# Kernel tuning notes

Hardware: AMD Instinct MI355X
Metric: run time of the kernel (lower is better)

## Reference

```python
import jax, jax.numpy as jnp
import numpy as np

B, S, D_IN, D_OUT, N, R = 8, 4096, 1280, 1280, 4, 16


def setup_inputs() -> dict:
    key = jax.random.key(0)
    ks = jax.random.split(key, 7)
    x = jax.random.normal(ks[0], (B, S, D_IN), dtype=jnp.float32)
    W = jax.random.normal(ks[1], (D_OUT, D_IN), dtype=jnp.float32) * 0.02
    bias = jax.random.normal(ks[2], (D_OUT,), dtype=jnp.float32) * 0.02
    A = jax.random.normal(ks[3], (N, R, D_IN), dtype=jnp.float32) * 0.02
    Bw = jax.random.normal(ks[4], (N, D_OUT, R), dtype=jnp.float32) * 0.02
    scalings = jax.random.uniform(ks[5], (N,), dtype=jnp.float32)
    masks = jax.random.uniform(ks[6], (N, S), dtype=jnp.float32)
    # normalize masks to sum ~1 per position, per docstring
    masks = masks / jnp.sum(masks, axis=0, keepdims=True)
    return {"x": x, "W": W, "bias": bias, "A": A, "Bw": Bw,
            "scalings": scalings, "masks": masks}


def reference(x, W, bias, A, Bw, scalings, masks):
    # base linear: y = x @ W^T + b
    base = jnp.einsum('bsd,od->bso', x, W) + bias
    # batched LoRA branches: h = x @ A_i^T  (b,s,n,r)
    h = jnp.einsum('bsd,nrd->bsnr', x, A)
    # lora_out_i = h @ B_i^T  (b,s,n,o)
    lora = jnp.einsum('bsnr,nor->bsno', h, Bw)
    # weighted sum over subjects: scaling_i * mask_i(pos)
    lora_sum = jnp.einsum('bsno,n,ns->bso', lora, scalings, masks)
    return base + lora_sum
```

## Files before the change

kernel.cpp:

```cpp
#include <hip/hip_runtime.h>
#include <hip/hip_bf16.h>
#include <stdint.h>

#define S_LEN   4096
#define DIN     1280
#define DOUT    1280
#define N_LORA  4
#define R_LORA  16
#define M_TOT   32768
#define KC      (DIN + N_LORA*R_LORA)
#define NR      64

typedef __attribute__((ext_vector_type(4))) float floatx4;
typedef __attribute__((ext_vector_type(8))) short shortx8;

typedef union { uint4 u; shortx8 s; } punx8;

static __device__ __forceinline__ unsigned short bf16_rne(float f) {
    union { float f; unsigned u; } v; v.f = f;
    unsigned u = v.u;
    u += 0x7fffu + ((u >> 16) & 1u);
    return (unsigned short)(u >> 16);
}

static __device__ __forceinline__ void async16(const unsigned short* g, unsigned short* l) {
    __builtin_amdgcn_global_load_lds(
        (const __attribute__((address_space(1))) unsigned int*)g,
        (__attribute__((address_space(3))) unsigned int*)l, 16, 0, 0);
}

static __device__ __forceinline__ uint4 cvt8(const float* src) {
    const float4* p = (const float4*)src;
    float4 a = p[0], b = p[1];
    uint4 o;
    o.x = (unsigned)bf16_rne(a.x) | ((unsigned)bf16_rne(a.y) << 16);
    o.y = (unsigned)bf16_rne(a.z) | ((unsigned)bf16_rne(a.w) << 16);
    o.z = (unsigned)bf16_rne(b.x) | ((unsigned)bf16_rne(b.y) << 16);
    o.w = (unsigned)bf16_rne(b.z) | ((unsigned)bf16_rne(b.w) << 16);
    return o;
}

__global__ __launch_bounds__(256) void k_convert_x(const float* __restrict__ x,
                                                   unsigned short* __restrict__ xb) {
    size_t e = ((size_t)blockIdx.x * 256 + threadIdx.x) * 8;
    *(uint4*)(xb + e) = cvt8(x + e);
}

__global__ __launch_bounds__(256) void k_build_wcat(const float* __restrict__ W,
                                                    const float* __restrict__ Bw,
                                                    unsigned short* __restrict__ Wcat) {
    int i = blockIdx.x * 256 + threadIdx.x;
    int e = i * 8;
    int o = e / KC;
    int c = e - o * KC;
    const float* src;
    if (c < DIN) {
        src = W + o * DIN + c;
    } else {
        int j = c - DIN;
        int n = j >> 4, r = j & 15;
        src = Bw + (n * DOUT + o) * R_LORA + r;
    }
    *(uint4*)(Wcat + o * KC + c) = cvt8(src);
}

__global__ __launch_bounds__(256) void k_convert_abp(const float* __restrict__ A,
                                                     unsigned short* __restrict__ Abp) {
    int step = blockIdx.x;
    int t = threadIdx.x;
    int ct = t >> 6, lane = t & 63;
    int mi = lane & 15, kq = lane >> 4;
    const float* src = A + (ct * 16 + mi) * DIN + step * 32 + kq * 8;
    *(uint4*)(Abp + ((size_t)(step * 4 + ct) * 64 + lane) * 8) = cvt8(src);
}

__global__ __launch_bounds__(1024) void k_lora_g(const unsigned short* __restrict__ xb,
                                                 const unsigned short* __restrict__ Abp,
                                                 const float* __restrict__ scalings,
                                                 const float* __restrict__ masks,
                                                 unsigned short* __restrict__ g) {
    __shared__ float hs[4][64][64];
    int tid = threadIdx.x;
    int wave = tid >> 6, lane = tid & 63;
    int kg = wave >> 2, wv = wave & 3;
    int mi = lane & 15, kq = lane >> 4;
    int m0 = blockIdx.x * 64;

    const unsigned short* xrow = xb + (size_t)(m0 + wv * 16 + mi) * DIN;

    floatx4 acc[4] = {};
    for (int s = 0; s < 10; ++s) {
        int step = kg * 10 + s;
        int k = step * 32 + kq * 8;
        shortx8 xf = *(const shortx8*)(xrow + k);
#pragma unroll
        for (int ct = 0; ct < 4; ++ct) {
            shortx8 bfr = *(const shortx8*)(Abp + ((size_t)(step * 4 + ct) * 64 + lane) * 8);
            acc[ct] = __builtin_amdgcn_mfma_f32_16x16x32_bf16(xf, bfr, acc[ct], 0, 0, 0);
        }
    }
#pragma unroll
    for (int ct = 0; ct < 4; ++ct)
#pragma unroll
        for (int reg = 0; reg < 4; ++reg)
            hs[kg][wv * 16 + kq * 4 + reg][ct * 16 + mi] = acc[ct][reg];
    __syncthreads();

    int r = tid >> 4;
    int c0 = (tid & 15) * 4;
    float4 s0 = *(const float4*)&hs[0][r][c0];
    float4 s1 = *(const float4*)&hs[1][r][c0];
    float4 s2 = *(const float4*)&hs[2][r][c0];
    float4 s3 = *(const float4*)&hs[3][r][c0];
    int n = c0 >> 4;
    int m = m0 + r;
    float wgt = scalings[n] * masks[n * S_LEN + (m & (S_LEN - 1))];
    float v0 = (s0.x + s1.x + s2.x + s3.x) * wgt;
    float v1 = (s0.y + s1.y + s2.y + s3.y) * wgt;
    float v2 = (s0.z + s1.z + s2.z + s3.z) * wgt;
    float v3 = (s0.w + s1.w + s2.w + s3.w) * wgt;
    uint2 packed;
    packed.x = (unsigned)bf16_rne(v0) | ((unsigned)bf16_rne(v1) << 16);
    packed.y = (unsigned)bf16_rne(v2) | ((unsigned)bf16_rne(v3) << 16);
    *(uint2*)(g + (size_t)m * NR + c0) = packed;
}

__global__ __launch_bounds__(256) void k_main_gemm(const unsigned short* __restrict__ xb,
                                                   const unsigned short* __restrict__ g,
                                                   const unsigned short* __restrict__ Wcat,
                                                   const float* __restrict__ bias,
                                                   float* __restrict__ out) {
    __shared__ unsigned short As[128 * 32];
    __shared__ unsigned short Bs[128 * 32];
    int tid = threadIdx.x;
    int wave = tid >> 6, lane = tid & 63;

    int bx = blockIdx.x;
    int xcd = bx & 7;
    int slot = bx >> 3;
    int rb = xcd * 32 + slot / 10;
    int cb = slot % 10;
    int m0 = rb * 128, n0 = cb * 128;

    int wr = wave >> 1, wc = wave & 1;
    int mi = lane & 15, kq = lane >> 4;

    int c0 = tid, c1 = tid + 256;
    int ar0 = c0 >> 2, ak0 = (c0 & 3) * 8;
    int ar1 = c1 >> 2, ak1 = (c1 & 3) * 8;

    floatx4 acc[4][4] = {};

    for (int k0 = 0; k0 < KC; k0 += 32) {
        if (k0 < DIN) {
            async16(xb + (size_t)(m0 + ar0) * DIN + k0 + ak0, As + c0 * 8);
            async16(xb + (size_t)(m0 + ar1) * DIN + k0 + ak1, As + c1 * 8);
        } else {
            async16(g + (size_t)(m0 + ar0) * NR + (k0 - DIN) + ak0, As + c0 * 8);
            async16(g + (size_t)(m0 + ar1) * NR + (k0 - DIN) + ak1, As + c1 * 8);
        }
        async16(Wcat + (size_t)(n0 + ar0) * KC + k0 + ak0, Bs + c0 * 8);
        async16(Wcat + (size_t)(n0 + ar1) * KC + k0 + ak1, Bs + c1 * 8);
        __syncthreads();
        shortx8 af[4], bf[4];
#pragma unroll
        for (int t = 0; t < 4; ++t) {
            af[t] = *(const shortx8*)(As + (wr * 64 + t * 16 + mi) * 32 + kq * 8);
            bf[t] = *(const shortx8*)(Bs + (wc * 64 + t * 16 + mi) * 32 + kq * 8);
        }
#pragma unroll
        for (int i = 0; i < 4; ++i)
#pragma unroll
            for (int j = 0; j < 4; ++j)
                acc[i][j] = __builtin_amdgcn_mfma_f32_16x16x32_bf16(af[i], bf[j], acc[i][j], 0, 0, 0);
        __syncthreads();
    }

#pragma unroll
    for (int j = 0; j < 4; ++j) {
        int col = n0 + wc * 64 + j * 16 + mi;
        float bv = bias[col];
#pragma unroll
        for (int i = 0; i < 4; ++i) {
            int rbase = m0 + wr * 64 + i * 16 + kq * 4;
#pragma unroll
            for (int reg = 0; reg < 4; ++reg) {
                out[(size_t)(rbase + reg) * DOUT + col] = acc[i][j][reg] + bv;
            }
        }
    }
}

extern "C" void kernel_launch(void* const* d_in, const int* in_sizes, int n_in,
                              void* d_out, int out_size, void* d_ws, size_t ws_size,
                              hipStream_t stream) {
    const float* x     = (const float*)d_in[0];
    const float* W     = (const float*)d_in[1];
    const float* bias  = (const float*)d_in[2];
    const float* A     = (const float*)d_in[3];
    const float* Bw    = (const float*)d_in[4];
    const float* scal  = (const float*)d_in[5];
    const float* masks = (const float*)d_in[6];
    float* out = (float*)d_out;

    unsigned short* xb   = (unsigned short*)d_ws;
    unsigned short* g    = xb + (size_t)M_TOT * DIN;
    unsigned short* Wcat = g + (size_t)M_TOT * NR;
    unsigned short* Abp  = Wcat + (size_t)DOUT * KC;

    k_convert_x<<<(M_TOT * DIN) / (8 * 256), 256, 0, stream>>>(x, xb);
    k_build_wcat<<<(DOUT * KC) / (8 * 256), 256, 0, stream>>>(W, Bw, Wcat);
    k_convert_abp<<<DIN / 32, 256, 0, stream>>>(A, Abp);
    k_lora_g<<<M_TOT / 64, 1024, 0, stream>>>(xb, Abp, scal, masks, g);
    k_main_gemm<<<(M_TOT / 128) * (DOUT / 128), 256, 0, stream>>>(xb, g, Wcat, bias, out);
}
```

Before: 465.8 us.

## Restructure main GEMM into double-buffered 256x128 tiles with swizzled LDS and split pipeline

The main GEMM moves from a 128x128 tile with 256 threads and single-buffered K=32 steps to a 256x128 tile with 512 threads, K=64 steps, and double-buffered LDS. Async global-to-LDS loads for the next tiles are issued between split MFMA phases, with explicit vmcnt waits, raw barriers and setprio, so memory traffic overlaps compute. LDS rows are XOR-swizzled to avoid bank conflicts on fragment reads. The larger per-block tile raises data reuse, but it also increases LDS use and register pressure, and the hand-written wait counts are fragile.

```diff
diff --git a/kernel.cpp b/kernel.cpp
--- a/kernel.cpp
+++ b/kernel.cpp
@@ -10,6 +10,7 @@
 #define M_TOT   32768
 #define KC      (DIN + N_LORA*R_LORA)
 #define NR      64
+#define NT      21
 
 typedef __attribute__((ext_vector_type(4))) float floatx4;
 typedef __attribute__((ext_vector_type(8))) short shortx8;
@@ -38,6 +39,13 @@
     o.z = (unsigned)bf16_rne(b.x) | ((unsigned)bf16_rne(b.y) << 16);
     o.w = (unsigned)bf16_rne(b.z) | ((unsigned)bf16_rne(b.w) << 16);
     return o;
+}
+
+#define VMCNT(n) asm volatile("s_waitcnt vmcnt(" #n ")" ::: "memory")
+static __device__ __forceinline__ void barx() {
+    asm volatile("" ::: "memory");
+    __builtin_amdgcn_s_barrier();
+    asm volatile("" ::: "memory");
 }
 
 __global__ __launch_bounds__(256) void k_convert_x(const float* __restrict__ x,
@@ -125,68 +133,126 @@
     *(uint2*)(g + (size_t)m * NR + c0) = packed;
 }
 
-__global__ __launch_bounds__(256) void k_main_gemm(const unsigned short* __restrict__ xb,
-                                                   const unsigned short* __restrict__ g,
-                                                   const unsigned short* __restrict__ Wcat,
-                                                   const float* __restrict__ bias,
-                                                   float* __restrict__ out) {
-    __shared__ unsigned short As[128 * 32];
-    __shared__ unsigned short Bs[128 * 32];
-    int tid = threadIdx.x;
-    int wave = tid >> 6, lane = tid & 63;
+__global__ __launch_bounds__(512, 2) void k_main_gemm(const unsigned short* __restrict__ xb,
+                                                      const unsigned short* __restrict__ g,
+                                                      const unsigned short* __restrict__ Wcat,
+                                                      const float* __restrict__ bias,
+                                                      float* __restrict__ out) {
+    __shared__ alignas(16) unsigned short As[2][256 * 64];
+    __shared__ alignas(16) unsigned short Bs[2][128 * 64];
+
+    const int tid = threadIdx.x;
+    const int wave = tid >> 6, lane = tid & 63;
+    const int wm = wave >> 1, wn = wave & 1;
+    const int mi = lane & 15, kq = lane >> 4;
 
     int bx = blockIdx.x;
-    int xcd = bx & 7;
-    int slot = bx >> 3;
-    int rb = xcd * 32 + slot / 10;
-    int cb = slot % 10;
-    int m0 = rb * 128, n0 = cb * 128;
-
-    int wr = wave >> 1, wc = wave & 1;
-    int mi = lane & 15, kq = lane >> 4;
-
-    int c0 = tid, c1 = tid + 256;
-    int ar0 = c0 >> 2, ak0 = (c0 & 3) * 8;
-    int ar1 = c1 >> 2, ak1 = (c1 & 3) * 8;
+    int xcd = bx & 7, slot = bx >> 3;
+    int srb = slot / 10;
+    const int m0 = (xcd * 16 + srb) * 256;
+    const int n0 = (slot - srb * 10) * 128;
+
+    const int tr = tid >> 3;
+    const int ts = (tid & 7) ^ (tr & 7);
+
+    const int sw  = (mi & 7) << 4;
+    const int cA  = (wm * 64 + mi) * 128;
+    const int cB  = (wn * 64 + mi) * 128;
+    const int co0 = (kq * 16) ^ sw;
+    const int co1 = (64 + kq * 16) ^ sw;
 
     floatx4 acc[4][4] = {};
 
-    for (int k0 = 0; k0 < KC; k0 += 32) {
-        if (k0 < DIN) {
-            async16(xb + (size_t)(m0 + ar0) * DIN + k0 + ak0, As + c0 * 8);
-            async16(xb + (size_t)(m0 + ar1) * DIN + k0 + ak1, As + c1 * 8);
-        } else {
-            async16(g + (size_t)(m0 + ar0) * NR + (k0 - DIN) + ak0, As + c0 * 8);
-            async16(g + (size_t)(m0 + ar1) * NR + (k0 - DIN) + ak1, As + c1 * 8);
-        }
-        async16(Wcat + (size_t)(n0 + ar0) * KC + k0 + ak0, Bs + c0 * 8);
-        async16(Wcat + (size_t)(n0 + ar1) * KC + k0 + ak1, Bs + c1 * 8);
-        __syncthreads();
-        shortx8 af[4], bf[4];
-#pragma unroll
-        for (int t = 0; t < 4; ++t) {
-            af[t] = *(const shortx8*)(As + (wr * 64 + t * 16 + mi) * 32 + kq * 8);
-            bf[t] = *(const shortx8*)(Bs + (wc * 64 + t * 16 + mi) * 32 + kq * 8);
-        }
-#pragma unroll
-        for (int i = 0; i < 4; ++i)
-#pragma unroll
-            for (int j = 0; j < 4; ++j)
-                acc[i][j] = __builtin_amdgcn_mfma_f32_16x16x32_bf16(af[i], bf[j], acc[i][j], 0, 0, 0);
-        __syncthreads();
-    }
-
-#pragma unroll
-    for (int j = 0; j < 4; ++j) {
-        int col = n0 + wc * 64 + j * 16 + mi;
+    auto stageA = [&](int t, int b) {
+#pragma unroll
+        for (int c = 0; c < 4; ++c) {
+            int r = c * 64 + tr;
+            const unsigned short* src = (t < 20)
+                ? xb + (size_t)(m0 + r) * DIN + t * 64 + ts * 8
+                : g  + (size_t)(m0 + r) * NR  + ts * 8;
+            async16(src, &As[b][(c * 512 + tid) * 8]);
+        }
+    };
+    auto stageB = [&](int t, int b) {
+#pragma unroll
+        for (int c = 0; c < 2; ++c) {
+            int r = c * 64 + tr;
+            async16(Wcat + (size_t)(n0 + r) * KC + t * 64 + ts * 8,
+                    &Bs[b][(c * 512 + tid) * 8]);
+        }
+    };
+
+    stageA(0, 0);
+    stageB(0, 0);
+    stageA(1, 1);
+    VMCNT(4);
+    barx();
+
+    for (int t = 0; t < NT; ++t) {
+        const int cur = t & 1;
+        const char* Ab = (const char*)As[cur];
+        const char* Bb = (const char*)Bs[cur];
+
+        shortx8 a[4][2], bfr[4][2];
+
+#pragma unroll
+        for (int f = 0; f < 4; ++f) {
+            const char* p = Ab + cA + f * (16 * 128);
+            a[f][0] = *(const shortx8*)(p + co0);
+            a[f][1] = *(const shortx8*)(p + co1);
+        }
+#pragma unroll
+        for (int nf = 0; nf < 2; ++nf) {
+            const char* p = Bb + cB + nf * (16 * 128);
+            bfr[nf][0] = *(const shortx8*)(p + co0);
+            bfr[nf][1] = *(const shortx8*)(p + co1);
+        }
+        if (t + 1 < NT) stageB(t + 1, cur ^ 1);
+        barx();
+        __builtin_amdgcn_s_setprio(1);
+#pragma unroll
+        for (int f = 0; f < 4; ++f)
+#pragma unroll
+            for (int nf = 0; nf < 2; ++nf) {
+                acc[f][nf] = __builtin_amdgcn_mfma_f32_16x16x32_bf16(a[f][0], bfr[nf][0], acc[f][nf], 0, 0, 0);
+                acc[f][nf] = __builtin_amdgcn_mfma_f32_16x16x32_bf16(a[f][1], bfr[nf][1], acc[f][nf], 0, 0, 0);
+            }
+        __builtin_amdgcn_s_setprio(0);
+        barx();
+
+#pragma unroll
+        for (int nf = 2; nf < 4; ++nf) {
+            const char* p = Bb + cB + nf * (16 * 128);
+            bfr[nf][0] = *(const shortx8*)(p + co0);
+            bfr[nf][1] = *(const shortx8*)(p + co1);
+        }
+        if (t + 2 < NT) stageA(t + 2, cur);
+        barx();
+        __builtin_amdgcn_s_setprio(1);
+#pragma unroll
+        for (int f = 0; f < 4; ++f)
+#pragma unroll
+            for (int nf = 2; nf < 4; ++nf) {
+                acc[f][nf] = __builtin_amdgcn_mfma_f32_16x16x32_bf16(a[f][0], bfr[nf][0], acc[f][nf], 0, 0, 0);
+                acc[f][nf] = __builtin_amdgcn_mfma_f32_16x16x32_bf16(a[f][1], bfr[nf][1], acc[f][nf], 0, 0, 0);
+            }
+        __builtin_amdgcn_s_setprio(0);
+        if (t < 19)      { VMCNT(4); }
+        else if (t == 19){ VMCNT(0); }
+        barx();
+    }
+
+#pragma unroll
+    for (int nf = 0; nf < 4; ++nf) {
+        int col = n0 + wn * 64 + nf * 16 + mi;
         float bv = bias[col];
 #pragma unroll
-        for (int i = 0; i < 4; ++i) {
-            int rbase = m0 + wr * 64 + i * 16 + kq * 4;
-#pragma unroll
-            for (int reg = 0; reg < 4; ++reg) {
-                out[(size_t)(rbase + reg) * DOUT + col] = acc[i][j][reg] + bv;
-            }
+        for (int f = 0; f < 4; ++f) {
+            int row = m0 + wm * 64 + f * 16 + kq * 4;
+            float* op = out + (size_t)row * DOUT + col;
+#pragma unroll
+            for (int reg = 0; reg < 4; ++reg)
+                op[(size_t)reg * DOUT] = acc[f][nf][reg] + bv;
         }
     }
 }
@@ -212,5 +278,5 @@
     k_build_wcat<<<(DOUT * KC) / (8 * 256), 256, 0, stream>>>(W, Bw, Wcat);
     k_convert_abp<<<DIN / 32, 256, 0, stream>>>(A, Abp);
     k_lora_g<<<M_TOT / 64, 1024, 0, stream>>>(xb, Abp, scal, masks, g);
-    k_main_gemm<<<(M_TOT / 128) * (DOUT / 128), 256, 0, stream>>>(xb, g, Wcat, bias, out);
-}
+    k_main_gemm<<<(M_TOT / 256) * (DOUT / 128), 512, 0, stream>>>(xb, g, Wcat, bias, out);
+}
```

After: 467.6 us. About the same (+0.4%).

## Rewrite main GEMM as 256x256 double-buffered, swizzled, interleaved-pipeline kernel

Applied to the files above, without the earlier changes.

The main bf16 GEMM moves from 128x128 tiles with K=32 and single-buffered LDS to 256x256 tiles with K=64, 512 threads and double-buffered LDS. The LDS layout is XOR-swizzled to avoid bank conflicts. Global-to-LDS async loads are interleaved with the MFMA phases using explicit vmcnt/lgkmcnt waits, barriers and setprio. This aims to hide memory latency and raise arithmetic intensity per tile. It relies on delicate manual wait counts, and the larger tiles give fewer blocks (640).

```diff
diff --git a/kernel.cpp b/kernel.cpp
--- a/kernel.cpp
+++ b/kernel.cpp
@@ -13,8 +13,6 @@
 
 typedef __attribute__((ext_vector_type(4))) float floatx4;
 typedef __attribute__((ext_vector_type(8))) short shortx8;
-
-typedef union { uint4 u; shortx8 s; } punx8;
 
 static __device__ __forceinline__ unsigned short bf16_rne(float f) {
     union { float f; unsigned u; } v; v.f = f;
@@ -38,6 +36,15 @@
     o.z = (unsigned)bf16_rne(b.x) | ((unsigned)bf16_rne(b.y) << 16);
     o.w = (unsigned)bf16_rne(b.z) | ((unsigned)bf16_rne(b.w) << 16);
     return o;
+}
+
+#define VMCNT(n) asm volatile("s_waitcnt vmcnt(" #n ")" ::: "memory")
+#define LGKM0    do { asm volatile("s_waitcnt lgkmcnt(0)" ::: "memory"); \
+                      __builtin_amdgcn_sched_barrier(0); } while (0)
+static __device__ __forceinline__ void barx() {
+    asm volatile("" ::: "memory");
+    __builtin_amdgcn_s_barrier();
+    asm volatile("" ::: "memory");
 }
 
 __global__ __launch_bounds__(256) void k_convert_x(const float* __restrict__ x,
@@ -125,70 +132,164 @@
     *(uint2*)(g + (size_t)m * NR + c0) = packed;
 }
 
-__global__ __launch_bounds__(256) void k_main_gemm(const unsigned short* __restrict__ xb,
-                                                   const unsigned short* __restrict__ g,
-                                                   const unsigned short* __restrict__ Wcat,
-                                                   const float* __restrict__ bias,
-                                                   float* __restrict__ out) {
-    __shared__ unsigned short As[128 * 32];
-    __shared__ unsigned short Bs[128 * 32];
-    int tid = threadIdx.x;
-    int wave = tid >> 6, lane = tid & 63;
+__global__ __launch_bounds__(512, 2) void k_main_gemm(const unsigned short* __restrict__ xb,
+                                                      const unsigned short* __restrict__ g,
+                                                      const unsigned short* __restrict__ Wcat,
+                                                      const float* __restrict__ bias,
+                                                      float* __restrict__ out) {
+    __shared__ alignas(16) unsigned short As[2][256 * 64];
+    __shared__ alignas(16) unsigned short Bs[2][256 * 64];
+
+    const int tid = threadIdx.x;
+    const int wave = tid >> 6, lane = tid & 63;
+    const int wm = wave >> 2, wn = wave & 3;
+    const int mi = lane & 15, kq = lane >> 4;
 
     int bx = blockIdx.x;
-    int xcd = bx & 7;
-    int slot = bx >> 3;
-    int rb = xcd * 32 + slot / 10;
-    int cb = slot % 10;
-    int m0 = rb * 128, n0 = cb * 128;
-
-    int wr = wave >> 1, wc = wave & 1;
-    int mi = lane & 15, kq = lane >> 4;
-
-    int c0 = tid, c1 = tid + 256;
-    int ar0 = c0 >> 2, ak0 = (c0 & 3) * 8;
-    int ar1 = c1 >> 2, ak1 = (c1 & 3) * 8;
-
-    floatx4 acc[4][4] = {};
-
-    for (int k0 = 0; k0 < KC; k0 += 32) {
-        if (k0 < DIN) {
-            async16(xb + (size_t)(m0 + ar0) * DIN + k0 + ak0, As + c0 * 8);
-            async16(xb + (size_t)(m0 + ar1) * DIN + k0 + ak1, As + c1 * 8);
+    int xcd = bx & 7, slot = bx >> 3;
+    int srb = slot / 5;
+    const int m0 = (xcd * 16 + srb) * 256;
+    const int n0 = (slot - srb * 5) * 256;
+
+    const int tr = tid >> 3;
+    const int ts = (tid & 7) ^ (tr & 7);
+
+    const unsigned short* pA = xb   + (size_t)(m0 + tr) * DIN + ts * 8;
+    const unsigned short* pG = g    + (size_t)(m0 + tr) * NR  + ts * 8;
+    const unsigned short* pB = Wcat + (size_t)(n0 + tr) * KC  + ts * 8;
+
+    const int swz  = mi & 7;
+    const int loK0 = mi * 128 + (((0) + kq) ^ swz) * 16;
+    const int loK1 = mi * 128 + (((4) + kq) ^ swz) * 16;
+    const int rbA  = (wm * 128) * 128;
+    const int rbB  = (wn * 64) * 128;
+
+    floatx4 acc[8][4] = {};
+    shortx8 a[8];
+    shortx8 b[2][4];
+
+    auto stA = [&](int t, int h) {
+        unsigned short* d = &As[t & 1][(h * 128) * 64 + tid * 8];
+        if (t < 20) {
+            const unsigned short* s = pA + (size_t)(h * 128) * DIN + t * 64;
+            async16(s, d);
+            async16(s + (size_t)64 * DIN, d + 64 * 64);
         } else {
-            async16(g + (size_t)(m0 + ar0) * NR + (k0 - DIN) + ak0, As + c0 * 8);
-            async16(g + (size_t)(m0 + ar1) * NR + (k0 - DIN) + ak1, As + c1 * 8);
+            const unsigned short* s = pG + (size_t)(h * 128) * NR;
+            async16(s, d);
+            async16(s + (size_t)64 * NR, d + 64 * 64);
         }
-        async16(Wcat + (size_t)(n0 + ar0) * KC + k0 + ak0, Bs + c0 * 8);
-        async16(Wcat + (size_t)(n0 + ar1) * KC + k0 + ak1, Bs + c1 * 8);
-        __syncthreads();
-        shortx8 af[4], bf[4];
-#pragma unroll
-        for (int t = 0; t < 4; ++t) {
-            af[t] = *(const shortx8*)(As + (wr * 64 + t * 16 + mi) * 32 + kq * 8);
-            bf[t] = *(const shortx8*)(Bs + (wc * 64 + t * 16 + mi) * 32 + kq * 8);
+    };
+    auto stB = [&](int t, int h) {
+        const unsigned short* s = pB + (size_t)(h * 128) * KC + t * 64;
+        unsigned short* d = &Bs[t & 1][(h * 128) * 64 + tid * 8];
+        async16(s, d);
+        async16(s + (size_t)64 * KC, d + 64 * 64);
+    };
+
+#define READ_A(bufb, mh)  _Pragma("unroll") \
+    for (int fm = 0; fm < 4; ++fm) { \
+        const char* p = (const char*)As[bufb] + rbA + ((mh) * 64 + fm * 16) * 128; \
+        a[fm * 2 + 0] = *(const shortx8*)(p + loK0); \
+        a[fm * 2 + 1] = *(const shortx8*)(p + loK1); \
+    }
+#define READ_B(bufb, nh)  _Pragma("unroll") \
+    for (int fn = 0; fn < 2; ++fn) { \
+        const char* p = (const char*)Bs[bufb] + rbB + ((nh) * 32 + fn * 16) * 128; \
+        b[nh][fn * 2 + 0] = *(const shortx8*)(p + loK0); \
+        b[nh][fn * 2 + 1] = *(const shortx8*)(p + loK1); \
+    }
+#define MFMA16(mh, nh)  do { __builtin_amdgcn_s_setprio(1); \
+    _Pragma("unroll") \
+    for (int fm = 0; fm < 4; ++fm) \
+        _Pragma("unroll") \
+        for (int fn = 0; fn < 2; ++fn) { \
+            acc[(mh)*4+fm][(nh)*2+fn] = __builtin_amdgcn_mfma_f32_16x16x32_bf16( \
+                a[fm*2+0], b[nh][fn*2+0], acc[(mh)*4+fm][(nh)*2+fn], 0, 0, 0); \
+            acc[(mh)*4+fm][(nh)*2+fn] = __builtin_amdgcn_mfma_f32_16x16x32_bf16( \
+                a[fm*2+1], b[nh][fn*2+1], acc[(mh)*4+fm][(nh)*2+fn], 0, 0, 0); \
+        } \
+    __builtin_amdgcn_s_setprio(0); } while (0)
+
+    stA(0, 0); stA(0, 1); stB(0, 0); stB(0, 1);
+    stB(1, 0); stB(1, 1); stA(1, 0);
+    VMCNT(6);
+    barx();
+
+    for (int it = 0; it < 10; ++it) {
+        const int T1 = 2 * it + 1, N0 = 2 * it + 2, N1 = 2 * it + 3;
+        const bool lastI = (it == 9);
+
+        READ_A(0, 0); READ_B(0, 0);
+        stA(T1, 1);
+        barx(); LGKM0;
+        MFMA16(0, 0);
+        barx();
+        READ_B(0, 1);
+        barx(); LGKM0;
+        MFMA16(0, 1);
+        barx();
+        READ_A(0, 1);
+        stB(N0, 0);
+        barx(); LGKM0;
+        MFMA16(1, 0);
+        barx();
+        stB(N0, 1); stA(N0, 0);
+        barx(); LGKM0;
+        MFMA16(1, 1);
+        VMCNT(6);
+        barx();
+        READ_A(1, 0); READ_B(1, 0);
+        stA(N0, 1);
+        barx(); LGKM0;
+        MFMA16(0, 0);
+        barx();
+        READ_B(1, 1);
+        barx(); LGKM0;
+        MFMA16(0, 1);
+        barx();
+        READ_A(1, 1);
+        if (!lastI) stB(N1, 0);
+        barx(); LGKM0;
+        MFMA16(1, 0);
+        barx();
+        if (!lastI) { stB(N1, 1); stA(N1, 0); }
+        barx(); LGKM0;
+        MFMA16(1, 1);
+        if (lastI) { VMCNT(0); } else { VMCNT(6); }
+        barx();
+    }
+
+    READ_A(0, 0); READ_B(0, 0);
+    LGKM0;
+    MFMA16(0, 0);
+    READ_B(0, 1);
+    LGKM0;
+    MFMA16(0, 1);
+    READ_A(0, 1);
+    LGKM0;
+    MFMA16(1, 0);
+    MFMA16(1, 1);
+
+    float bv[4];
+#pragma unroll
+    for (int nf = 0; nf < 4; ++nf)
+        bv[nf] = bias[n0 + wn * 64 + (nf >> 1) * 32 + (nf & 1) * 16 + mi];
+#pragma unroll
+    for (int mf = 0; mf < 8; ++mf) {
+        const int row = m0 + wm * 128 + (mf >> 2) * 64 + (mf & 3) * 16 + kq * 4;
+#pragma unroll
+        for (int nf = 0; nf < 4; ++nf) {
+            const int col = n0 + wn * 64 + (nf >> 1) * 32 + (nf & 1) * 16 + mi;
+            float* op = out + (size_t)row * DOUT + col;
+#pragma unroll
+            for (int reg = 0; reg < 4; ++reg)
+                op[(size_t)reg * DOUT] = acc[mf][nf][reg] + bv[nf];
         }
-#pragma unroll
-        for (int i = 0; i < 4; ++i)
-#pragma unroll
-            for (int j = 0; j < 4; ++j)
-                acc[i][j] = __builtin_amdgcn_mfma_f32_16x16x32_bf16(af[i], bf[j], acc[i][j], 0, 0, 0);
-        __syncthreads();
-    }
-
-#pragma unroll
-    for (int j = 0; j < 4; ++j) {
-        int col = n0 + wc * 64 + j * 16 + mi;
-        float bv = bias[col];
-#pragma unroll
-        for (int i = 0; i < 4; ++i) {
-            int rbase = m0 + wr * 64 + i * 16 + kq * 4;
-#pragma unroll
-            for (int reg = 0; reg < 4; ++reg) {
-                out[(size_t)(rbase + reg) * DOUT + col] = acc[i][j][reg] + bv;
-            }
-        }
-    }
+    }
+#undef READ_A
+#undef READ_B
+#undef MFMA16
 }
 
 extern "C" void kernel_launch(void* const* d_in, const int* in_sizes, int n_in,
@@ -212,5 +313,5 @@
     k_build_wcat<<<(DOUT * KC) / (8 * 256), 256, 0, stream>>>(W, Bw, Wcat);
     k_convert_abp<<<DIN / 32, 256, 0, stream>>>(A, Abp);
     k_lora_g<<<M_TOT / 64, 1024, 0, stream>>>(xb, Abp, scal, masks, g);
-    k_main_gemm<<<(M_TOT / 128) * (DOUT / 128), 256, 0, stream>>>(xb, g, Wcat, bias, out);
-}
+    k_main_gemm<<<(M_TOT / 256) * (DOUT / 256), 512, 0, stream>>>(xb, g, Wcat, bias, out);
+}
```

New measurement: 434.8 us. 1.07x faster.
